# Performance work log

Hardware: AMD Instinct MI355X
Metric: run time of the kernel (lower is better)

Reference implementation:

```python
import jax, jax.numpy as jnp
import numpy as np
import math

D_MODEL = 768
N_HEADS = 12
D_HEAD = D_MODEL // N_HEADS
B, T = 2, 2048
EPS = 1e-5


def _layernorm(x, g, b):
    mu = jnp.mean(x, axis=-1, keepdims=True)
    var = jnp.var(x, axis=-1, keepdims=True)
    return (x - mu) * jax.lax.rsqrt(var + EPS) * g + b


def setup_inputs() -> dict:
    key = jax.random.key(0)
    ks = jax.random.split(key, 16)
    s = 0.02
    inp = {
        "x": jax.random.normal(ks[0], (B, T, D_MODEL), jnp.float32),
        "q_pos": jax.random.normal(ks[1], (B, N_HEADS, T, D_HEAD), jnp.float32),
        "k_pos": jax.random.normal(ks[2], (B, N_HEADS, T, D_HEAD), jnp.float32),
        "causal_mask": jnp.triu(jnp.ones((T, T), dtype=bool), k=1),
        "Wq": jax.random.normal(ks[3], (D_MODEL, D_MODEL), jnp.float32) * s,
        "bq": jnp.zeros((D_MODEL,), jnp.float32),
        "Wk": jax.random.normal(ks[4], (D_MODEL, D_MODEL), jnp.float32) * s,
        "bk": jnp.zeros((D_MODEL,), jnp.float32),
        "Wv": jax.random.normal(ks[5], (D_MODEL, D_MODEL), jnp.float32) * s,
        "bv": jnp.zeros((D_MODEL,), jnp.float32),
        "Wo": jax.random.normal(ks[6], (D_MODEL, D_MODEL), jnp.float32) * s,
        "bo": jnp.zeros((D_MODEL,), jnp.float32),
        "ln1_g": jnp.ones((D_MODEL,), jnp.float32),
        "ln1_b": jnp.zeros((D_MODEL,), jnp.float32),
        "ln2_g": jnp.ones((D_MODEL,), jnp.float32),
        "ln2_b": jnp.zeros((D_MODEL,), jnp.float32),
        "W1": jax.random.normal(ks[7], (D_MODEL, 4 * D_MODEL), jnp.float32) * s,
        "b1": jnp.zeros((4 * D_MODEL,), jnp.float32),
        "W2": jax.random.normal(ks[8], (4 * D_MODEL, D_MODEL), jnp.float32) * s,
        "b2": jnp.zeros((D_MODEL,), jnp.float32),
    }
    return inp


def reference(x, q_pos, k_pos, causal_mask, Wq, bq, Wk, bk, Wv, bv, Wo, bo,
              ln1_g, ln1_b, ln2_g, ln2_b, W1, b1, W2, b2):
    h = _layernorm(x, ln1_g, ln1_b)  # [B,T,D]
    # project and split heads -> [B,H,T,d]
    def heads(y):
        return y.reshape(B, T, N_HEADS, D_HEAD).transpose(0, 2, 1, 3)
    Qc = heads(h @ Wq + bq)
    Kc = heads(h @ Wk + bk)
    V = heads(h @ Wv + bv)
    scale = math.sqrt(D_HEAD)
    A_X = jnp.einsum('bhqd,bhkd->bhqk', Qc, Kc) / scale
    A_P = jnp.einsum('bhqd,bhkd->bhqk', q_pos, k_pos) / scale
    scores = A_X * A_P  # Hadamard combination of content + positional scores
    scores = jnp.where(causal_mask[None, None, :, :], -jnp.inf, scores)
    attn = jax.nn.softmax(scores, axis=-1)
    out = jnp.einsum('bhqk,bhkd->bhqd', attn, V)  # [B,H,T,d]
    out = out.transpose(0, 2, 1, 3).reshape(B, T, D_MODEL)
    out = out @ Wo + bo
    x = x + out
    h2 = _layernorm(x, ln2_g, ln2_b)
    ffn = jax.nn.gelu(h2 @ W1 + b1, approximate=False) @ W2 + b2
    return x + ffn
```

## Files before the change

### kernel.cpp

```cpp
#include <hip/hip_runtime.h>
#include <hip/hip_bf16.h>
#include <math.h>

#define D_MODEL 768
#define N_HEADS 12
#define D_HEAD  64
#define BATCH   2
#define SEQ     2048
#define ROWS    (BATCH*SEQ)
#define D_FFN   (4*D_MODEL)

typedef short bf16x8 __attribute__((ext_vector_type(8)));
typedef float f32x4  __attribute__((ext_vector_type(4)));

__device__ __forceinline__ short f2bf(float f) {
    __hip_bfloat16 h = __float2bfloat16(f);
    return *reinterpret_cast<short*>(&h);
}

template<int CTRL>
__device__ __forceinline__ float dpp_f(float x) {
    int v = __builtin_amdgcn_update_dpp(0, __float_as_int(x), CTRL, 0xF, 0xF, true);
    return __int_as_float(v);
}
__device__ __forceinline__ float dpp_max16(float x) {
    x = fmaxf(x, dpp_f<0xB1>(x));
    x = fmaxf(x, dpp_f<0x4E>(x));
    x = fmaxf(x, dpp_f<0x141>(x));
    x = fmaxf(x, dpp_f<0x140>(x));
    return x;
}
__device__ __forceinline__ float dpp_sum16(float x) {
    x += dpp_f<0xB1>(x);
    x += dpp_f<0x4E>(x);
    x += dpp_f<0x141>(x);
    x += dpp_f<0x140>(x);
    return x;
}

__global__ __launch_bounds__(256)
void prep_kernel(const float* __restrict__ Wq, const float* __restrict__ Wk,
                 const float* __restrict__ Wv, const float* __restrict__ Wo,
                 const float* __restrict__ W1, const float* __restrict__ W2,
                 const float* __restrict__ q_pos, const float* __restrict__ k_pos,
                 short* __restrict__ WTq, short* __restrict__ WTk,
                 short* __restrict__ WTv, short* __restrict__ WTo,
                 short* __restrict__ WT1, short* __restrict__ WT2,
                 short* __restrict__ qp_bf, short* __restrict__ kp_bf) {
    int id = blockIdx.x;
    if (id >= 6912) {
        int cid = id - 6912;
        bool isq = (cid < 1536);
        int c = isq ? cid : cid - 1536;
        const float* src = isq ? q_pos : k_pos;
        short* dst = isq ? qp_bf : kp_bf;
        float sc = isq ? 0.125f : 1.0f;
        int i = (c * 256 + threadIdx.x) * 8;
        float4 a = *reinterpret_cast<const float4*>(src + i);
        float4 b = *reinterpret_cast<const float4*>(src + i + 4);
        bf16x8 r;
        r[0]=f2bf(a.x*sc); r[1]=f2bf(a.y*sc); r[2]=f2bf(a.z*sc); r[3]=f2bf(a.w*sc);
        r[4]=f2bf(b.x*sc); r[5]=f2bf(b.y*sc); r[6]=f2bf(b.z*sc); r[7]=f2bf(b.w*sc);
        *reinterpret_cast<bf16x8*>(dst + i) = r;
        return;
    }
    const float* W; short* WT; int K, N, t;
    if (id < 576)        { W = Wq; WT = WTq; K = 768;  N = 768;  t = id; }
    else if (id < 1152)  { W = Wk; WT = WTk; K = 768;  N = 768;  t = id - 576; }
    else if (id < 1728)  { W = Wv; WT = WTv; K = 768;  N = 768;  t = id - 1152; }
    else if (id < 2304)  { W = Wo; WT = WTo; K = 768;  N = 768;  t = id - 1728; }
    else if (id < 4608)  { W = W1; WT = WT1; K = 768;  N = 3072; t = id - 2304; }
    else                 { W = W2; WT = WT2; K = 3072; N = 768;  t = id - 4608; }
    int nb = N >> 5;
    int n0 = (t % nb) * 32, k0 = (t / nb) * 32;
    __shared__ float tile[32][33];
    int tx = threadIdx.x & 31, ty = threadIdx.x >> 5;
    #pragma unroll
    for (int i = 0; i < 4; ++i)
        tile[ty + 8*i][tx] = W[(size_t)(k0 + ty + 8*i) * N + n0 + tx];
    __syncthreads();
    #pragma unroll
    for (int i = 0; i < 4; ++i)
        WT[(size_t)(n0 + ty + 8*i) * K + k0 + tx] = f2bf(tile[tx][ty + 8*i]);
}

__global__ __launch_bounds__(256)
void transpose_v_kernel(const short* __restrict__ Vm, short* __restrict__ Vt) {
    __shared__ short tile[64][72];
    int kt = blockIdx.x;
    int bh = blockIdx.y;
    int b = bh / N_HEADS, h = bh % N_HEADS;
    int tid = threadIdx.x;
    int row = tid >> 2, c16 = (tid & 3) * 16;
    const short* src = Vm + ((size_t)(b * SEQ) + kt * 64 + row) * D_MODEL + h * 64 + c16;
    *reinterpret_cast<bf16x8*>(&tile[row][c16])     = *reinterpret_cast<const bf16x8*>(src);
    *reinterpret_cast<bf16x8*>(&tile[row][c16 + 8]) = *reinterpret_cast<const bf16x8*>(src + 8);
    __syncthreads();
    int d = tid >> 2, k16 = (tid & 3) * 16;
    short o[16];
    #pragma unroll
    for (int j = 0; j < 16; ++j) o[j] = tile[k16 + j][d];
    short* dst = Vt + ((size_t)bh * 64 + d) * SEQ + kt * 64 + k16;
    *reinterpret_cast<bf16x8*>(dst)     = *reinterpret_cast<bf16x8*>(&o[0]);
    *reinterpret_cast<bf16x8*>(dst + 8) = *reinterpret_cast<bf16x8*>(&o[8]);
}

__global__ __launch_bounds__(256)
void ln_kernel(const float* __restrict__ x, const float* __restrict__ g,
               const float* __restrict__ beta, short* __restrict__ out) {
    int row = blockIdx.x;
    const float* xr = x + (size_t)row * D_MODEL;
    int t = threadIdx.x;
    float v0 = xr[t], v1 = xr[t + 256], v2 = xr[t + 512];
    float s  = v0 + v1 + v2;
    float s2 = v0*v0 + v1*v1 + v2*v2;
    __shared__ float rs[4], rs2[4];
    #pragma unroll
    for (int off = 32; off; off >>= 1) {
        s  += __shfl_down(s, off);
        s2 += __shfl_down(s2, off);
    }
    int wv = t >> 6, ln = t & 63;
    if (ln == 0) { rs[wv] = s; rs2[wv] = s2; }
    __syncthreads();
    float S  = rs[0] + rs[1] + rs[2] + rs[3];
    float S2 = rs2[0] + rs2[1] + rs2[2] + rs2[3];
    float mu  = S * (1.0f / D_MODEL);
    float var = S2 * (1.0f / D_MODEL) - mu * mu;
    float inv = rsqrtf(var + 1e-5f);
    short* orow = out + (size_t)row * D_MODEL;
    orow[t]       = f2bf((v0 - mu) * inv * g[t]       + beta[t]);
    orow[t + 256] = f2bf((v1 - mu) * inv * g[t + 256] + beta[t + 256]);
    orow[t + 512] = f2bf((v2 - mu) * inv * g[t + 512] + beta[t + 512]);
}

template<int ACT, bool RES, bool OUTBF>
__device__ __forceinline__
void gemm_body(const short* __restrict__ A, const short* __restrict__ WT,
               const float* __restrict__ bias, const float* __restrict__ res,
               void* __restrict__ Cout, int M, int N, int Kloop, int Kstride,
               float oscale) {
    __shared__ short As[2][128 * 32];
    __shared__ short Bs[2][128 * 32];
    const int tid = threadIdx.x;
    const int w = tid >> 6, lane = tid & 63;
    const int lr = lane & 15, lg = lane >> 4;
    const int wm = w >> 1, wn = w & 1;
    const int bm = blockIdx.y * 128, bn = blockIdx.x * 128;

    f32x4 acc[4][4] = {};

    const int srow = w * 32 + (lane >> 2);
    const int scol = (lane & 3) * 8;
    const short* Ag = A  + (size_t)(bm + srow) * Kstride + scol;
    const short* Bg = WT + (size_t)(bn + srow) * Kstride + scol;

    auto stage = [&](int k0, int buf) {
        #pragma unroll
        for (int r = 0; r < 2; ++r) {
            __builtin_amdgcn_global_load_lds(
                (const __attribute__((address_space(1))) void*)(Ag + (size_t)r * 16 * Kstride + k0),
                (__attribute__((address_space(3))) void*)(&As[buf][0] + w * 1024 + r * 512),
                16, 0, 0);
            __builtin_amdgcn_global_load_lds(
                (const __attribute__((address_space(1))) void*)(Bg + (size_t)r * 16 * Kstride + k0),
                (__attribute__((address_space(3))) void*)(&Bs[buf][0] + w * 1024 + r * 512),
                16, 0, 0);
        }
    };

    stage(0, 0);
    __syncthreads();
    int cur = 0;

    for (int k0 = 0; k0 < Kloop; k0 += 32) {
        if (k0 + 32 < Kloop) stage(k0 + 32, cur ^ 1);

        bf16x8 af[4], bfr[4];
        #pragma unroll
        for (int mi = 0; mi < 4; ++mi)
            af[mi] = *reinterpret_cast<const bf16x8*>(&As[cur][0] + (wm*64 + mi*16 + lr) * 32 + lg*8);
        #pragma unroll
        for (int nj = 0; nj < 4; ++nj)
            bfr[nj] = *reinterpret_cast<const bf16x8*>(&Bs[cur][0] + (wn*64 + nj*16 + lr) * 32 + lg*8);
        __builtin_amdgcn_s_setprio(1);
        #pragma unroll
        for (int mi = 0; mi < 4; ++mi)
            #pragma unroll
            for (int nj = 0; nj < 4; ++nj)
                acc[mi][nj] = __builtin_amdgcn_mfma_f32_16x16x32_bf16(af[mi], bfr[nj], acc[mi][nj], 0, 0, 0);
        __builtin_amdgcn_s_setprio(0);

        __syncthreads();
        cur ^= 1;
    }

    float bias_v[4] = {0.f, 0.f, 0.f, 0.f};
    if constexpr (ACT != 2) {
        #pragma unroll
        for (int nj = 0; nj < 4; ++nj) bias_v[nj] = bias[bn + wn*64 + nj*16 + lr];
    }

    #pragma unroll
    for (int mi = 0; mi < 4; ++mi) {
        #pragma unroll
        for (int j = 0; j < 4; ++j) {
            size_t m = bm + wm*64 + mi*16 + lg*4 + j;
            #pragma unroll
            for (int nj = 0; nj < 4; ++nj) {
                size_t n = bn + wn*64 + nj*16 + lr;
                float v = acc[mi][nj][j] + bias_v[nj];
                if (RES) v += res[m * N + n];
                if (ACT == 1) v = 0.5f * v * (1.0f + erff(v * 0.70710678118f));
                if (OUTBF) ((short*)Cout)[m * N + n] = f2bf(v * oscale);
                else       ((float*)Cout)[m * N + n] = v;
            }
        }
    }
}

template<int ACT, bool RES, bool OUTBF>
__global__ __launch_bounds__(256)
void gemm_mfma_kernel(const short* __restrict__ A, const short* __restrict__ WT,
                      const float* __restrict__ bias, const float* __restrict__ res,
                      void* __restrict__ Cout, int M, int N, int K) {
    gemm_body<ACT, RES, OUTBF>(A, WT, bias, res, Cout, M, N, K, K, 1.0f);
}

__global__ __launch_bounds__(256)
void gemm_qkv_kernel(const short* __restrict__ A,
                     const short* __restrict__ WTq, const short* __restrict__ WTk,
                     const short* __restrict__ WTv,
                     const float* __restrict__ bq, const float* __restrict__ bk,
                     const float* __restrict__ bv,
                     short* __restrict__ Qm, short* __restrict__ Km, short* __restrict__ Vm) {
    const short* WT; const float* bias; short* C; float sc;
    if (blockIdx.z == 0)      { WT = WTq; bias = bq; C = Qm; sc = 0.125f; }
    else if (blockIdx.z == 1) { WT = WTk; bias = bk; C = Km; sc = 1.0f; }
    else                      { WT = WTv; bias = bv; C = Vm; sc = 1.0f; }
    gemm_body<0, false, true>(A, WT, bias, nullptr, C, ROWS, D_MODEL, D_MODEL, D_MODEL, sc);
}

__global__ __launch_bounds__(256)
void gemm_w2_kernel(const short* __restrict__ mid, const short* __restrict__ WT2,
                    float* __restrict__ P0, float* __restrict__ P1) {
    int z = blockIdx.z;
    gemm_body<2, false, false>(mid + z * 1536, WT2 + z * 1536, nullptr, nullptr,
                               z ? P1 : P0, ROWS, D_MODEL, 1536, D_FFN, 1.0f);
}

__global__ __launch_bounds__(256)
void w2_epi_kernel(const float* __restrict__ P0, const float* __restrict__ P1,
                   const float* __restrict__ b2, const float* __restrict__ x2,
                   float* __restrict__ out) {
    size_t i = ((size_t)blockIdx.x * 256 + threadIdx.x) * 4;
    int n = (int)(i % D_MODEL);
    float4 p0 = *reinterpret_cast<const float4*>(P0 + i);
    float4 p1 = *reinterpret_cast<const float4*>(P1 + i);
    float4 xr = *reinterpret_cast<const float4*>(x2 + i);
    float4 bb = *reinterpret_cast<const float4*>(b2 + n);
    float4 o;
    o.x = p0.x + p1.x + xr.x + bb.x;
    o.y = p0.y + p1.y + xr.y + bb.y;
    o.z = p0.z + p1.z + xr.z + bb.z;
    o.w = p0.w + p1.w + xr.w + bb.w;
    *reinterpret_cast<float4*>(out + i) = o;
}

__global__ __launch_bounds__(128)
void attn_mfma_kernel(const short* __restrict__ Q, const short* __restrict__ K,
                      const short* __restrict__ Vt, const short* __restrict__ qp,
                      const short* __restrict__ kp, short* __restrict__ ao) {
    __shared__ short Ks[2][4096];
    __shared__ short kps[2][4096];
    __shared__ short Vts[2][4096];
    __shared__ short Plds[2][16][72];

    int lin = blockIdx.x;
    int wid = (lin & 7) * 96 + (lin >> 3);
    int bh = wid >> 5;
    int pair = wid & 31;
    int b = bh / N_HEADS, h = bh % N_HEADS;
    int tid = threadIdx.x, w = tid >> 6, lane = tid & 63;
    int lr = lane & 15, lg = lane >> 4;

    const short* Kh  = K  + (size_t)(b * SEQ) * D_MODEL + h * 64;
    const short* kph = kp + (size_t)bh * SEQ * 64;
    const short* Vth = Vt + (size_t)bh * 64 * SEQ;

    const int s_sub  = lane >> 3;
    const int s_colb = ((lane & 7) ^ s_sub) << 4;

    auto stage = [&](int kt, int buf) {
        #pragma unroll
        for (int j = 0; j < 4; ++j) {
            int row = (w * 4 + j) * 8 + s_sub;
            int ldsoff = (w * 4 + j) * 1024;
            __builtin_amdgcn_global_load_lds(
                (const __attribute__((address_space(1))) void*)
                    ((const char*)(Kh + (size_t)(kt * 64 + row) * D_MODEL) + s_colb),
                (__attribute__((address_space(3))) void*)((char*)&Ks[buf][0] + ldsoff), 16, 0, 0);
            __builtin_amdgcn_global_load_lds(
                (const __attribute__((address_space(1))) void*)
                    ((const char*)(kph + (size_t)(kt * 64 + row) * 64) + s_colb),
                (__attribute__((address_space(3))) void*)((char*)&kps[buf][0] + ldsoff), 16, 0, 0);
            __builtin_amdgcn_global_load_lds(
                (const __attribute__((address_space(1))) void*)
                    ((const char*)(Vth + (size_t)row * SEQ + kt * 64) + s_colb),
                (__attribute__((address_space(3))) void*)((char*)&Vts[buf][0] + ldsoff), 16, 0, 0);
        }
    };
    auto ldr = [&](const short* base, int row, int halfb) -> bf16x8 {
        int off = row * 128 + ((halfb + lg * 16) ^ ((row & 7) << 4));
        return *reinterpret_cast<const bf16x8*>((const char*)base + off);
    };

    #pragma unroll
    for (int ph = 0; ph < 2; ++ph) {
        int qt = ph ? 63 - pair : pair;
        int qbase = qt * 32 + w * 16;

        const short* Qrow  = Q  + ((size_t)(b * SEQ) + qbase + lr) * D_MODEL + h * 64;
        const short* qprow = qp + ((size_t)bh * SEQ + qbase + lr) * 64;
        bf16x8 qf0  = *reinterpret_cast<const bf16x8*>(Qrow + lg * 8);
        bf16x8 qf1  = *reinterpret_cast<const bf16x8*>(Qrow + 32 + lg * 8);
        bf16x8 qpf0 = *reinterpret_cast<const bf16x8*>(qprow + lg * 8);
        bf16x8 qpf1 = *reinterpret_cast<const bf16x8*>(qprow + 32 + lg * 8);

        f32x4 o_acc[4] = {};
        float m_run[4], l_run[4];
        #pragma unroll
        for (int r = 0; r < 4; ++r) { m_run[r] = -1e30f; l_run[r] = 0.f; }

        int nkt = qt / 2 + 1;
        stage(0, 0);
        __syncthreads();
        int cur = 0;

        for (int kt = 0; kt < nkt; ++kt) {
            if (kt + 1 < nkt) stage(kt + 1, cur ^ 1);

            const short* Kb  = &Ks[cur][0];
            const short* kpb = &kps[cur][0];
            const short* Vb  = &Vts[cur][0];
            f32x4 sx[4] = {}, sp[4] = {};
            __builtin_amdgcn_s_setprio(1);
            #pragma unroll
            for (int sub = 0; sub < 4; ++sub) {
                int row = sub * 16 + lr;
                bf16x8 kf0 = ldr(Kb, row, 0),  kf1 = ldr(Kb, row, 64);
                bf16x8 kq0 = ldr(kpb, row, 0), kq1 = ldr(kpb, row, 64);
                sx[sub] = __builtin_amdgcn_mfma_f32_16x16x32_bf16(qf0,  kf0, sx[sub], 0, 0, 0);
                sx[sub] = __builtin_amdgcn_mfma_f32_16x16x32_bf16(qf1,  kf1, sx[sub], 0, 0, 0);
                sp[sub] = __builtin_amdgcn_mfma_f32_16x16x32_bf16(qpf0, kq0, sp[sub], 0, 0, 0);
                sp[sub] = __builtin_amdgcn_mfma_f32_16x16x32_bf16(qpf1, kq1, sp[sub], 0, 0, 0);
            }
            __builtin_amdgcn_s_setprio(0);

            float sc[4][4];
            float pmax[4];
            bool diag = (kt == nkt - 1);
            #pragma unroll
            for (int r = 0; r < 4; ++r) {
                int row = qbase + lg * 4 + r;
                float mx = -1e30f;
                #pragma unroll
                for (int sub = 0; sub < 4; ++sub) {
                    float v = sx[sub][r] * sp[sub][r];
                    if (diag) {
                        int col = kt * 64 + sub * 16 + lr;
                        if (col > row) v = -1e30f;
                    }
                    sc[sub][r] = v;
                    mx = fmaxf(mx, v);
                }
                pmax[r] = dpp_max16(mx);
            }

            bool need = false;
            #pragma unroll
            for (int r = 0; r < 4; ++r) need = need || (pmax[r] > m_run[r] + 8.f);
            if (__any(need)) {
                #pragma unroll
                for (int r = 0; r < 4; ++r) {
                    float m_new = fmaxf(m_run[r], pmax[r]);
                    float scale = __expf(m_run[r] - m_new);
                    m_run[r] = m_new;
                    l_run[r] *= scale;
                    #pragma unroll
                    for (int ds = 0; ds < 4; ++ds) o_acc[ds][r] *= scale;
                }
            }
            #pragma unroll
            for (int r = 0; r < 4; ++r) {
                float s = 0.f;
                #pragma unroll
                for (int sub = 0; sub < 4; ++sub) {
                    float pv = __expf(sc[sub][r] - m_run[r]);
                    sc[sub][r] = pv;
                    s += pv;
                }
                l_run[r] += dpp_sum16(s);
            }

            #pragma unroll
            for (int sub = 0; sub < 4; ++sub)
                #pragma unroll
                for (int r = 0; r < 4; ++r)
                    Plds[w][lg * 4 + r][sub * 16 + lr] = f2bf(sc[sub][r]);

            bf16x8 pa0 = *reinterpret_cast<bf16x8*>(&Plds[w][lr][lg * 8]);
            bf16x8 pa1 = *reinterpret_cast<bf16x8*>(&Plds[w][lr][32 + lg * 8]);

            __builtin_amdgcn_s_setprio(1);
            #pragma unroll
            for (int ds = 0; ds < 4; ++ds) {
                int row = ds * 16 + lr;
                bf16x8 vb0 = ldr(Vb, row, 0), vb1 = ldr(Vb, row, 64);
                o_acc[ds] = __builtin_amdgcn_mfma_f32_16x16x32_bf16(pa0, vb0, o_acc[ds], 0, 0, 0);
                o_acc[ds] = __builtin_amdgcn_mfma_f32_16x16x32_bf16(pa1, vb1, o_acc[ds], 0, 0, 0);
            }
            __builtin_amdgcn_s_setprio(0);

            __syncthreads();
            cur ^= 1;
        }

        #pragma unroll
        for (int ds = 0; ds < 4; ++ds)
            #pragma unroll
            for (int r = 0; r < 4; ++r) {
                int row = qbase + lg * 4 + r;
                float val = o_acc[ds][r] / l_run[r];
                ao[((size_t)(b * SEQ) + row) * D_MODEL + h * 64 + ds * 16 + lr] = f2bf(val);
            }
        __syncthreads();
    }
}

extern "C" void kernel_launch(void* const* d_in, const int* in_sizes, int n_in,
                              void* d_out, int out_size, void* d_ws, size_t ws_size,
                              hipStream_t stream) {
    const float* x     = (const float*)d_in[0];
    const float* q_pos = (const float*)d_in[1];
    const float* k_pos = (const float*)d_in[2];
    const float* Wq = (const float*)d_in[4];
    const float* bq = (const float*)d_in[5];
    const float* Wk = (const float*)d_in[6];
    const float* bk = (const float*)d_in[7];
    const float* Wv = (const float*)d_in[8];
    const float* bv = (const float*)d_in[9];
    const float* Wo = (const float*)d_in[10];
    const float* bo = (const float*)d_in[11];
    const float* ln1_g = (const float*)d_in[12];
    const float* ln1_b = (const float*)d_in[13];
    const float* ln2_g = (const float*)d_in[14];
    const float* ln2_b = (const float*)d_in[15];
    const float* W1 = (const float*)d_in[16];
    const float* b1 = (const float*)d_in[17];
    const float* W2 = (const float*)d_in[18];
    const float* b2 = (const float*)d_in[19];
    float* out = (float*)d_out;

    char* p = (char*)d_ws;
    auto alloc = [&](size_t bytes) { char* q = p; p += (bytes + 255) & ~(size_t)255; return q; };
    const size_t SA = (size_t)ROWS * D_MODEL;
    const size_t SP = (size_t)BATCH * N_HEADS * SEQ * 64;

    short* h_bf  = (short*)alloc(SA * 2);
    short* Qm    = (short*)alloc(SA * 2);
    short* Km    = (short*)alloc(SA * 2);
    short* Vm    = (short*)alloc(SA * 2);
    short* Vt    = (short*)alloc(SP * 2);
    short* ao    = (short*)alloc(SA * 2);
    short* qp_bf = (short*)alloc(SP * 2);
    short* kp_bf = (short*)alloc(SP * 2);
    short* mid   = (short*)alloc((size_t)ROWS * D_FFN * 2);
    float* x2    = (float*)alloc(SA * 4);
    float* P0    = (float*)alloc(SA * 4);
    float* P1    = (float*)alloc(SA * 4);
    short* WTq   = (short*)alloc((size_t)D_MODEL * D_MODEL * 2);
    short* WTk   = (short*)alloc((size_t)D_MODEL * D_MODEL * 2);
    short* WTv   = (short*)alloc((size_t)D_MODEL * D_MODEL * 2);
    short* WTo   = (short*)alloc((size_t)D_MODEL * D_MODEL * 2);
    short* WT1   = (short*)alloc((size_t)D_MODEL * D_FFN * 2);
    short* WT2   = (short*)alloc((size_t)D_MODEL * D_FFN * 2);

    prep_kernel<<<9984, 256, 0, stream>>>(Wq, Wk, Wv, Wo, W1, W2, q_pos, k_pos,
                                          WTq, WTk, WTv, WTo, WT1, WT2, qp_bf, kp_bf);

    ln_kernel<<<ROWS, 256, 0, stream>>>(x, ln1_g, ln1_b, h_bf);
    gemm_qkv_kernel<<<dim3(D_MODEL/128, ROWS/128, 3), 256, 0, stream>>>(
        h_bf, WTq, WTk, WTv, bq, bk, bv, Qm, Km, Vm);
    transpose_v_kernel<<<dim3(SEQ/64, BATCH*N_HEADS), 256, 0, stream>>>(Vm, Vt);
    attn_mfma_kernel<<<768, 128, 0, stream>>>(Qm, Km, Vt, qp_bf, kp_bf, ao);
    gemm_mfma_kernel<0, true, false><<<dim3(D_MODEL/128, ROWS/128), 256, 0, stream>>>(
        ao, WTo, bo, x, x2, ROWS, D_MODEL, D_MODEL);
    ln_kernel<<<ROWS, 256, 0, stream>>>(x2, ln2_g, ln2_b, h_bf);
    gemm_mfma_kernel<1, false, true><<<dim3(D_FFN/128, ROWS/128), 256, 0, stream>>>(
        h_bf, WT1, b1, nullptr, mid, ROWS, D_FFN, D_MODEL);
    gemm_w2_kernel<<<dim3(D_MODEL/128, ROWS/128, 2), 256, 0, stream>>>(mid, WT2, P0, P1);
    w2_epi_kernel<<<(int)(SA/1024), 256, 0, stream>>>(P0, P1, b2, x2, out);
}
```

Measured before the change: 229.1 us.

## Split-K the Wo GEMM, fuse residual into LN2, fold LN1 into prep

The output projection now runs as a two-way split-K GEMM, writing partial sums to P0/P1, which doubles the block count from 192 to 384. The bias, residual add and partial-sum reduction are folded into the second layernorm kernel, which also writes x2. The first layernorm is merged into the prep kernel as extra blocks, removing one launch, and the attention P buffer's LDS padding changes from 72 to 76. The trade-off is extra fp32 partial-sum traffic to global memory and a gemm_body template used with ACT=2 for the Wo path.

```diff
diff --git a/kernel.cpp b/kernel.cpp
--- a/kernel.cpp
+++ b/kernel.cpp
@@ -43,11 +43,41 @@
                  const float* __restrict__ Wv, const float* __restrict__ Wo,
                  const float* __restrict__ W1, const float* __restrict__ W2,
                  const float* __restrict__ q_pos, const float* __restrict__ k_pos,
+                 const float* __restrict__ x, const float* __restrict__ ln1_g,
+                 const float* __restrict__ ln1_b,
                  short* __restrict__ WTq, short* __restrict__ WTk,
                  short* __restrict__ WTv, short* __restrict__ WTo,
                  short* __restrict__ WT1, short* __restrict__ WT2,
-                 short* __restrict__ qp_bf, short* __restrict__ kp_bf) {
+                 short* __restrict__ qp_bf, short* __restrict__ kp_bf,
+                 short* __restrict__ h_bf) {
     int id = blockIdx.x;
+    if (id >= 9984) {
+        int row = id - 9984;
+        const float* xr = x + (size_t)row * D_MODEL;
+        int t = threadIdx.x;
+        float v0 = xr[t], v1 = xr[t + 256], v2 = xr[t + 512];
+        float s  = v0 + v1 + v2;
+        float s2 = v0*v0 + v1*v1 + v2*v2;
+        __shared__ float rs[4], rs2[4];
+        #pragma unroll
+        for (int off = 32; off; off >>= 1) {
+            s  += __shfl_down(s, off);
+            s2 += __shfl_down(s2, off);
+        }
+        int wv = t >> 6, ln = t & 63;
+        if (ln == 0) { rs[wv] = s; rs2[wv] = s2; }
+        __syncthreads();
+        float S  = rs[0] + rs[1] + rs[2] + rs[3];
+        float S2 = rs2[0] + rs2[1] + rs2[2] + rs2[3];
+        float mu  = S * (1.0f / D_MODEL);
+        float var = S2 * (1.0f / D_MODEL) - mu * mu;
+        float inv = rsqrtf(var + 1e-5f);
+        short* orow = h_bf + (size_t)row * D_MODEL;
+        orow[t]       = f2bf((v0 - mu) * inv * ln1_g[t]       + ln1_b[t]);
+        orow[t + 256] = f2bf((v1 - mu) * inv * ln1_g[t + 256] + ln1_b[t + 256]);
+        orow[t + 512] = f2bf((v2 - mu) * inv * ln1_g[t + 512] + ln1_b[t + 512]);
+        return;
+    }
     if (id >= 6912) {
         int cid = id - 6912;
         bool isq = (cid < 1536);
@@ -106,12 +136,17 @@
 }
 
 __global__ __launch_bounds__(256)
-void ln_kernel(const float* __restrict__ x, const float* __restrict__ g,
-               const float* __restrict__ beta, short* __restrict__ out) {
+void ln2_fuse_kernel(const float* __restrict__ P0, const float* __restrict__ P1,
+                     const float* __restrict__ bo, const float* __restrict__ x,
+                     const float* __restrict__ g, const float* __restrict__ beta,
+                     float* __restrict__ x2, short* __restrict__ out) {
     int row = blockIdx.x;
-    const float* xr = x + (size_t)row * D_MODEL;
+    size_t base = (size_t)row * D_MODEL;
     int t = threadIdx.x;
-    float v0 = xr[t], v1 = xr[t + 256], v2 = xr[t + 512];
+    float v0 = P0[base + t]       + P1[base + t]       + bo[t]       + x[base + t];
+    float v1 = P0[base + t + 256] + P1[base + t + 256] + bo[t + 256] + x[base + t + 256];
+    float v2 = P0[base + t + 512] + P1[base + t + 512] + bo[t + 512] + x[base + t + 512];
+    x2[base + t] = v0; x2[base + t + 256] = v1; x2[base + t + 512] = v2;
     float s  = v0 + v1 + v2;
     float s2 = v0*v0 + v1*v1 + v2*v2;
     __shared__ float rs[4], rs2[4];
@@ -128,7 +163,7 @@
     float mu  = S * (1.0f / D_MODEL);
     float var = S2 * (1.0f / D_MODEL) - mu * mu;
     float inv = rsqrtf(var + 1e-5f);
-    short* orow = out + (size_t)row * D_MODEL;
+    short* orow = out + base;
     orow[t]       = f2bf((v0 - mu) * inv * g[t]       + beta[t]);
     orow[t + 256] = f2bf((v1 - mu) * inv * g[t + 256] + beta[t + 256]);
     orow[t + 512] = f2bf((v2 - mu) * inv * g[t + 512] + beta[t + 512]);
@@ -239,6 +274,14 @@
     else if (blockIdx.z == 1) { WT = WTk; bias = bk; C = Km; sc = 1.0f; }
     else                      { WT = WTv; bias = bv; C = Vm; sc = 1.0f; }
     gemm_body<0, false, true>(A, WT, bias, nullptr, C, ROWS, D_MODEL, D_MODEL, D_MODEL, sc);
+}
+
+__global__ __launch_bounds__(256)
+void gemm_wo_kernel(const short* __restrict__ ao, const short* __restrict__ WTo,
+                    float* __restrict__ P0, float* __restrict__ P1) {
+    int z = blockIdx.z;
+    gemm_body<2, false, false>(ao + z * 384, WTo + z * 384, nullptr, nullptr,
+                               z ? P1 : P0, ROWS, D_MODEL, 384, D_MODEL, 1.0f);
 }
 
 __global__ __launch_bounds__(256)
@@ -274,7 +317,7 @@
     __shared__ short Ks[2][4096];
     __shared__ short kps[2][4096];
     __shared__ short Vts[2][4096];
-    __shared__ short Plds[2][16][72];
+    __shared__ short Plds[2][16][76];
 
     int lin = blockIdx.x;
     int wid = (lin & 7) * 96 + (lin >> 3);
@@ -486,17 +529,17 @@
     short* WT1   = (short*)alloc((size_t)D_MODEL * D_FFN * 2);
     short* WT2   = (short*)alloc((size_t)D_MODEL * D_FFN * 2);
 
-    prep_kernel<<<9984, 256, 0, stream>>>(Wq, Wk, Wv, Wo, W1, W2, q_pos, k_pos,
-                                          WTq, WTk, WTv, WTo, WT1, WT2, qp_bf, kp_bf);
-
-    ln_kernel<<<ROWS, 256, 0, stream>>>(x, ln1_g, ln1_b, h_bf);
+    prep_kernel<<<14080, 256, 0, stream>>>(Wq, Wk, Wv, Wo, W1, W2, q_pos, k_pos,
+                                           x, ln1_g, ln1_b,
+                                           WTq, WTk, WTv, WTo, WT1, WT2,
+                                           qp_bf, kp_bf, h_bf);
+
     gemm_qkv_kernel<<<dim3(D_MODEL/128, ROWS/128, 3), 256, 0, stream>>>(
         h_bf, WTq, WTk, WTv, bq, bk, bv, Qm, Km, Vm);
     transpose_v_kernel<<<dim3(SEQ/64, BATCH*N_HEADS), 256, 0, stream>>>(Vm, Vt);
     attn_mfma_kernel<<<768, 128, 0, stream>>>(Qm, Km, Vt, qp_bf, kp_bf, ao);
-    gemm_mfma_kernel<0, true, false><<<dim3(D_MODEL/128, ROWS/128), 256, 0, stream>>>(
-        ao, WTo, bo, x, x2, ROWS, D_MODEL, D_MODEL);
-    ln_kernel<<<ROWS, 256, 0, stream>>>(x2, ln2_g, ln2_b, h_bf);
+    gemm_wo_kernel<<<dim3(D_MODEL/128, ROWS/128, 2), 256, 0, stream>>>(ao, WTo, P0, P1);
+    ln2_fuse_kernel<<<ROWS, 256, 0, stream>>>(P0, P1, bo, x, ln2_g, ln2_b, x2, h_bf);
     gemm_mfma_kernel<1, false, true><<<dim3(D_FFN/128, ROWS/128), 256, 0, stream>>>(
         h_bf, WT1, b1, nullptr, mid, ROWS, D_FFN, D_MODEL);
     gemm_w2_kernel<<<dim3(D_MODEL/128, ROWS/128, 2), 256, 0, stream>>>(mid, WT2, P0, P1);
```

Result: slower. 259.0 us (+13.1%).
